# Kernel optimization log

Hardware: AMD Instinct MI355X
Metric: run time of the kernel (lower is better)

Reference implementation:

```python
import jax, jax.numpy as jnp
import numpy as np

B, L, D, H, NL, NR, FF = 4, 512, 1024, 8, 2, 37, 4096
DH = D // H  # 128, relation embedding dim (shared across heads, per RAT-SQL)


def layer_norm(x, g, b, eps=1e-5):
    m = jnp.mean(x, axis=-1, keepdims=True)
    v = jnp.mean(jnp.square(x - m), axis=-1, keepdims=True)
    return (x - m) * jax.lax.rsqrt(v + eps) * g + b


def setup_inputs() -> dict:
    key = jax.random.key(0)
    ks = iter(jax.random.split(key, 24))

    def p(shape, scale=0.02):
        return jax.random.normal(next(ks), shape, jnp.float32) * scale

    return {
        "x": jax.random.normal(next(ks), (B, L, D), jnp.float32),
        "relations": jax.random.randint(next(ks), (B, L, L), 0, NR),
        "Wq": p((NL, D, D)), "bq": jnp.zeros((NL, D), jnp.float32),
        "Wk": p((NL, D, D)), "bk": jnp.zeros((NL, D), jnp.float32),
        "Wv": p((NL, D, D)), "bv": jnp.zeros((NL, D), jnp.float32),
        "Wo": p((NL, D, D)), "bo": jnp.zeros((NL, D), jnp.float32),
        "rel_k": p((NL, NR, DH)), "rel_v": p((NL, NR, DH)),
        "W1": p((NL, D, FF)), "b1": jnp.zeros((NL, FF), jnp.float32),
        "W2": p((NL, FF, D)), "b2": jnp.zeros((NL, D), jnp.float32),
        "ln1_g": jnp.ones((NL, D), jnp.float32), "ln1_b": jnp.zeros((NL, D), jnp.float32),
        "ln2_g": jnp.ones((NL, D), jnp.float32), "ln2_b": jnp.zeros((NL, D), jnp.float32),
        "lnf_g": jnp.ones((D,), jnp.float32), "lnf_b": jnp.zeros((D,), jnp.float32),
    }


def reference(x, relations, Wq, bq, Wk, bk, Wv, bv, Wo, bo, rel_k, rel_v,
              W1, b1, W2, b2, ln1_g, ln1_b, ln2_g, ln2_b, lnf_g, lnf_b):
    scale = jnp.float32(1.0 / np.sqrt(DH))

    def split_heads(t):  # [B,L,D] -> [B,H,L,DH]
        return t.reshape(B, L, H, DH).transpose(0, 2, 1, 3)

    for l in range(NL):
        # --- relation-aware multi-head attention (pre-norm sublayer) ---
        h = layer_norm(x, ln1_g[l], ln1_b[l])
        q = split_heads(h @ Wq[l] + bq[l])
        k = split_heads(h @ Wk[l] + bk[l])
        v = split_heads(h @ Wv[l] + bv[l])
        rk = rel_k[l][relations]  # [B,L,L,DH] gathered relation key embeddings
        rv = rel_v[l][relations]  # [B,L,L,DH]
        scores = (jnp.einsum('bhid,bhjd->bhij', q, k)
                  + jnp.einsum('bhid,bijd->bhij', q, rk)) * scale
        attn = jax.nn.softmax(scores, axis=-1)  # [B,H,L,L]
        o = (jnp.einsum('bhij,bhjd->bhid', attn, v)
             + jnp.einsum('bhij,bijd->bhid', attn, rv))
        o = o.transpose(0, 2, 1, 3).reshape(B, L, D) @ Wo[l] + bo[l]
        x = x + o
        # --- feed-forward sublayer (pre-norm) ---
        h2 = layer_norm(x, ln2_g[l], ln2_b[l])
        x = x + jax.nn.relu(h2 @ W1[l] + b1[l]) @ W2[l] + b2[l]
    return layer_norm(x, lnf_g, lnf_b)
```

## Files before the change

kernel.cpp:

```cpp
#include <hip/hip_runtime.h>

#define Bdim 4
#define Ldim 512
#define Ddim 1024
#define Hdim 8
#define NLdim 2
#define NRdim 37
#define FFdim 4096
#define DHdim 128
#define ROWS 2048

using bf16x8 = __attribute__((ext_vector_type(8))) short;
using s16x4  = __attribute__((ext_vector_type(4))) short;
using s16x8  = __attribute__((ext_vector_type(8))) short;
using f32x4  = __attribute__((ext_vector_type(4))) float;

struct HL { short h, l; };
__device__ __forceinline__ HL splitf(float f) {
    HL r;
    unsigned u = __float_as_uint(f);
    unsigned rh = (u + 0x7FFFu + ((u >> 16) & 1u)) >> 16;
    r.h = (short)rh;
    float res = f - __uint_as_float(rh << 16);
    unsigned v = __float_as_uint(res);
    r.l = (short)((v + 0x7FFFu + ((v >> 16) & 1u)) >> 16);
    return r;
}

__device__ __forceinline__ size_t ssa_off(int row, int k, int KK) {
    return (size_t)row * KK + (k & ~63) + (((((k >> 3) & 7) ^ (row & 7))) << 3) + (k & 7);
}

__device__ __forceinline__ void gload16(const void* g, void* l) {
    __builtin_amdgcn_global_load_lds(
        (const __attribute__((address_space(1))) void*)g,
        (__attribute__((address_space(3))) void*)l, 16, 0, 0);
}

template<bool SPLIT>
__global__ __launch_bounds__(256) void ln_kernel(
    const float* __restrict__ x, const float* __restrict__ g,
    const float* __restrict__ beta, float* __restrict__ outf,
    short* __restrict__ oh, short* __restrict__ ol)
{
    int row = blockIdx.x;
    int t = threadIdx.x;
    const float4* xr = (const float4*)(x + (size_t)row * Ddim);
    float4 v = xr[t];
    float s  = v.x + v.y + v.z + v.w;
    float ss = v.x*v.x + v.y*v.y + v.z*v.z + v.w*v.w;
    #pragma unroll
    for (int off = 32; off; off >>= 1) {
        s  += __shfl_down(s, off);
        ss += __shfl_down(ss, off);
    }
    __shared__ float rs[4], rss[4], stat[2];
    int wave = t >> 6, lane = t & 63;
    if (lane == 0) { rs[wave] = s; rss[wave] = ss; }
    __syncthreads();
    if (t == 0) {
        float a = rs[0] + rs[1] + rs[2] + rs[3];
        float b = rss[0] + rss[1] + rss[2] + rss[3];
        float mean = a * (1.0f / Ddim);
        float var  = b * (1.0f / Ddim) - mean * mean;
        stat[0] = mean;
        stat[1] = rsqrtf(var + 1e-5f);
    }
    __syncthreads();
    float mean = stat[0], inv = stat[1];
    float4 gv = ((const float4*)g)[t];
    float4 bv = ((const float4*)beta)[t];
    float4 o;
    o.x = (v.x - mean) * inv * gv.x + bv.x;
    o.y = (v.y - mean) * inv * gv.y + bv.y;
    o.z = (v.z - mean) * inv * gv.z + bv.z;
    o.w = (v.w - mean) * inv * gv.w + bv.w;
    if (SPLIT) {
        int d = t * 4;
        size_t off = ssa_off(row, d, Ddim);
        HL a0 = splitf(o.x), a1 = splitf(o.y), a2 = splitf(o.z), a3 = splitf(o.w);
        s16x4 hv, lv;
        hv[0] = a0.h; hv[1] = a1.h; hv[2] = a2.h; hv[3] = a3.h;
        lv[0] = a0.l; lv[1] = a1.l; lv[2] = a2.l; lv[3] = a3.l;
        *(s16x4*)&oh[off] = hv;
        *(s16x4*)&ol[off] = lv;
    } else {
        ((float4*)(outf + (size_t)row * Ddim))[t] = o;
    }
}

__global__ __launch_bounds__(256) void prep_w(
    const float* __restrict__ W, short* __restrict__ oh, short* __restrict__ ol,
    int N, int logN)
{
    int gi = blockIdx.x * 256 + threadIdx.x;
    int n = gi & (N - 1);
    int rest = gi >> logN;
    int g = rest & 7, kt = rest >> 3;
    const float* src = W + ((size_t)(kt * 64 + g * 8)) * N + n;
    s16x8 h8, l8;
    #pragma unroll
    for (int j = 0; j < 8; ++j) {
        HL a = splitf(src[(size_t)j * N]);
        h8[j] = a.h; l8[j] = a.l;
    }
    size_t off = ((size_t)kt * N + n) * 64 + (((g ^ (n & 7))) << 3);
    *(s16x8*)&oh[off] = h8;
    *(s16x8*)&ol[off] = l8;
}

struct G3 {
    const short* Wh[3]; const short* Wl[3];
    const float* bias[3];
    float* outf[3];
    short* oh[3]; short* ol[3];
};

template<bool RES, bool RELU, bool SPLIT>
__global__ __launch_bounds__(256) void gemm3(
    const short* __restrict__ Ahi, const short* __restrict__ Alo,
    const float* __restrict__ res, G3 gp, int N, int K)
{
    __shared__ __align__(16) short As_h[128 * 64];
    __shared__ __align__(16) short As_l[128 * 64];
    __shared__ __align__(16) short Ws_h[64 * 64];
    __shared__ __align__(16) short Ws_l[64 * 64];

    int z = blockIdx.z;
    const short* Wh = gp.Wh[z];
    const short* Wl = gp.Wl[z];
    const float* bias = gp.bias[z];

    int t = threadIdx.x, wid = t >> 6, lane = t & 63;
    int bm = blockIdx.y * 128, bn = blockIdx.x * 64;
    int wr = wid >> 1, wc = wid & 1;

    f32x4 acc[4][2];
    #pragma unroll
    for (int m = 0; m < 4; ++m)
        #pragma unroll
        for (int n = 0; n < 2; ++n)
            acc[m][n] = (f32x4)(0.f);

    int nkt = K >> 6;
    int l8r = lane >> 3, l8c = lane & 7;

    for (int kt = 0; kt < nkt; ++kt) {
        size_t kof = (size_t)kt * 64 + l8c * 8;
        #pragma unroll
        for (int qq = 0; qq < 4; ++qq) {
            int rb = wid * 32 + qq * 8;
            gload16(Ahi + (size_t)(bm + rb + l8r) * K + kof, &As_h[rb * 64]);
            gload16(Alo + (size_t)(bm + rb + l8r) * K + kof, &As_l[rb * 64]);
        }
        size_t wbase = (size_t)kt * N * 64;
        #pragma unroll
        for (int qq = 0; qq < 2; ++qq) {
            int nb = wid * 16 + qq * 8;
            gload16(Wh + wbase + (size_t)(bn + nb + l8r) * 64 + l8c * 8, &Ws_h[nb * 64]);
            gload16(Wl + wbase + (size_t)(bn + nb + l8r) * 64 + l8c * 8, &Ws_l[nb * 64]);
        }
        __syncthreads();
        #pragma unroll
        for (int ks = 0; ks < 2; ++ks) {
            int kg = ks * 4 + (lane >> 4);
            int sw = (kg ^ (lane & 7)) << 3;
            bf16x8 ah[4], al[4], bh[2], bl[2];
            #pragma unroll
            for (int m = 0; m < 4; ++m) {
                int off = (wr * 64 + m * 16 + (lane & 15)) * 64 + sw;
                ah[m] = *(const bf16x8*)&As_h[off];
                al[m] = *(const bf16x8*)&As_l[off];
            }
            #pragma unroll
            for (int n = 0; n < 2; ++n) {
                int off = (wc * 32 + n * 16 + (lane & 15)) * 64 + sw;
                bh[n] = *(const bf16x8*)&Ws_h[off];
                bl[n] = *(const bf16x8*)&Ws_l[off];
            }
            #pragma unroll
            for (int m = 0; m < 4; ++m)
                #pragma unroll
                for (int n = 0; n < 2; ++n) {
                    acc[m][n] = __builtin_amdgcn_mfma_f32_16x16x32_bf16(ah[m], bh[n], acc[m][n], 0, 0, 0);
                    acc[m][n] = __builtin_amdgcn_mfma_f32_16x16x32_bf16(ah[m], bl[n], acc[m][n], 0, 0, 0);
                    acc[m][n] = __builtin_amdgcn_mfma_f32_16x16x32_bf16(al[m], bh[n], acc[m][n], 0, 0, 0);
                }
        }
        __syncthreads();
    }

    int r0 = (lane >> 4) << 2, cl = lane & 15;
    #pragma unroll
    for (int m = 0; m < 4; ++m) {
        #pragma unroll
        for (int n = 0; n < 2; ++n) {
            int col = bn + wc * 32 + n * 16 + cl;
            float bia = bias[col];
            #pragma unroll
            for (int j = 0; j < 4; ++j) {
                int row = bm + wr * 64 + m * 16 + r0 + j;
                float val = acc[m][n][j] + bia;
                if (RES) val += res[(size_t)row * N + col];
                if (RELU) val = fmaxf(val, 0.f);
                if (SPLIT) {
                    HL a = splitf(val);
                    size_t o = ssa_off(row, col, N);
                    gp.oh[z][o] = a.h;
                    gp.ol[z][o] = a.l;
                } else {
                    gp.outf[z][(size_t)row * N + col] = val;
                }
            }
        }
    }
}

__global__ __launch_bounds__(256) void qr_kernel(
    const float* __restrict__ q, const float* __restrict__ relk,
    float* __restrict__ qr)
{
    __shared__ __align__(16) float qrow[Ddim];
    __shared__ float rkT[DHdim][NRdim + 3];
    int bi = blockIdx.x, t = threadIdx.x;
    ((float4*)qrow)[t] = ((const float4*)(q + (size_t)bi * Ddim))[t];
    for (int idx = t; idx < NRdim * DHdim; idx += 256) {
        int r = idx >> 7, d = idx & 127;
        rkT[d][r] = relk[idx];
    }
    __syncthreads();
    for (int o = t; o < Hdim * NRdim; o += 256) {
        int h = o / NRdim, r = o - h * NRdim;
        const float* qp = qrow + h * DHdim;
        float acc = 0.f;
        #pragma unroll 4
        for (int d = 0; d < DHdim; ++d)
            acc = fmaf(qp[d], rkT[d][r], acc);
        qr[(size_t)bi * (Hdim * NRdim) + o] = acc;
    }
}

__global__ __launch_bounds__(256) void attn_kernel(
    const float* __restrict__ q, const float* __restrict__ k,
    const float* __restrict__ v, const int* __restrict__ relations,
    const float* __restrict__ qr, const float* __restrict__ relv,
    short* __restrict__ o_hi, short* __restrict__ o_lo)
{
    __shared__ __align__(16) float Qs[32][132];
    __shared__ __align__(16) float Ks[32][132];
    __shared__ __align__(16) float Vs[32][132];
    __shared__ float Ps[32][36];
    __shared__ float aw[32][40];

    int t = threadIdx.x;
    int blk = blockIdx.x;
    int it = blk & 15, bh = blk >> 4;
    int h = bh & 7, b = bh >> 3;
    int i0 = it * 32;
    int r = t >> 3, q8 = t & 7;
    int row_g = b * Ldim + i0 + r;

    const float* qrow = q + (size_t)row_g * Ddim + h * DHdim;
    #pragma unroll
    for (int c = 0; c < 4; ++c)
        *(float4*)&Qs[r][q8 * 16 + c * 4] = *(const float4*)&qrow[q8 * 16 + c * 4];
    for (int idx = t; idx < 32 * 40; idx += 256) ((float*)aw)[idx] = 0.f;

    const int*   relp = relations + (size_t)row_g * Ldim;
    const float* qrp  = qr + (size_t)row_g * (Hdim * NRdim) + h * NRdim;

    float4 oc0 = make_float4(0,0,0,0), oc1 = oc0, oc2 = oc0, oc3 = oc0;
    float mrun = -1e30f, lsum = 0.f;
    const float scale = 0.08838834764831845f;

    for (int jt = 0; jt < 16; ++jt) {
        int j0 = jt * 32;
        __syncthreads();
        const float* krow = k + (size_t)(b * Ldim + j0 + r) * Ddim + h * DHdim;
        const float* vrow = v + (size_t)(b * Ldim + j0 + r) * Ddim + h * DHdim;
        #pragma unroll
        for (int c = 0; c < 4; ++c) {
            *(float4*)&Ks[r][q8 * 16 + c * 4] = *(const float4*)&krow[q8 * 16 + c * 4];
            *(float4*)&Vs[r][q8 * 16 + c * 4] = *(const float4*)&vrow[q8 * 16 + c * 4];
        }
        __syncthreads();

        float s0 = 0.f, s1 = 0.f, s2 = 0.f, s3 = 0.f;
        #pragma unroll 8
        for (int dq = 0; dq < 32; ++dq) {
            float4 qv = *(const float4*)&Qs[r][dq * 4];
            float4 k0 = *(const float4*)&Ks[q8     ][dq * 4];
            float4 k1 = *(const float4*)&Ks[q8 +  8][dq * 4];
            float4 k2 = *(const float4*)&Ks[q8 + 16][dq * 4];
            float4 k3 = *(const float4*)&Ks[q8 + 24][dq * 4];
            s0 = fmaf(qv.x, k0.x, s0); s0 = fmaf(qv.y, k0.y, s0); s0 = fmaf(qv.z, k0.z, s0); s0 = fmaf(qv.w, k0.w, s0);
            s1 = fmaf(qv.x, k1.x, s1); s1 = fmaf(qv.y, k1.y, s1); s1 = fmaf(qv.z, k1.z, s1); s1 = fmaf(qv.w, k1.w, s1);
            s2 = fmaf(qv.x, k2.x, s2); s2 = fmaf(qv.y, k2.y, s2); s2 = fmaf(qv.z, k2.z, s2); s2 = fmaf(qv.w, k2.w, s2);
            s3 = fmaf(qv.x, k3.x, s3); s3 = fmaf(qv.y, k3.y, s3); s3 = fmaf(qv.z, k3.z, s3); s3 = fmaf(qv.w, k3.w, s3);
        }
        int rel0 = relp[j0 + q8];
        int rel1 = relp[j0 + q8 + 8];
        int rel2 = relp[j0 + q8 + 16];
        int rel3 = relp[j0 + q8 + 24];
        s0 = (s0 + qrp[rel0]) * scale;
        s1 = (s1 + qrp[rel1]) * scale;
        s2 = (s2 + qrp[rel2]) * scale;
        s3 = (s3 + qrp[rel3]) * scale;

        float mt = fmaxf(fmaxf(s0, s1), fmaxf(s2, s3));
        mt = fmaxf(mt, __shfl_xor(mt, 1));
        mt = fmaxf(mt, __shfl_xor(mt, 2));
        mt = fmaxf(mt, __shfl_xor(mt, 4));
        float mnew = fmaxf(mrun, mt);
        float corr = __expf(mrun - mnew);
        mrun = mnew;
        float p0 = __expf(s0 - mnew);
        float p1 = __expf(s1 - mnew);
        float p2 = __expf(s2 - mnew);
        float p3 = __expf(s3 - mnew);
        lsum = lsum * corr + (p0 + p1 + p2 + p3);
        oc0.x *= corr; oc0.y *= corr; oc0.z *= corr; oc0.w *= corr;
        oc1.x *= corr; oc1.y *= corr; oc1.z *= corr; oc1.w *= corr;
        oc2.x *= corr; oc2.y *= corr; oc2.z *= corr; oc2.w *= corr;
        oc3.x *= corr; oc3.y *= corr; oc3.z *= corr; oc3.w *= corr;
        for (int ri = q8; ri < NRdim; ri += 8) aw[r][ri] *= corr;
        atomicAdd(&aw[r][rel0], p0);
        atomicAdd(&aw[r][rel1], p1);
        atomicAdd(&aw[r][rel2], p2);
        atomicAdd(&aw[r][rel3], p3);
        Ps[r][q8]      = p0;
        Ps[r][q8 + 8]  = p1;
        Ps[r][q8 + 16] = p2;
        Ps[r][q8 + 24] = p3;

        #pragma unroll 4
        for (int j = 0; j < 32; ++j) {
            float p = Ps[r][j];
            float4 v0 = *(const float4*)&Vs[j][(q8     ) * 4];
            float4 v1 = *(const float4*)&Vs[j][(q8 +  8) * 4];
            float4 v2 = *(const float4*)&Vs[j][(q8 + 16) * 4];
            float4 v3 = *(const float4*)&Vs[j][(q8 + 24) * 4];
            oc0.x = fmaf(p, v0.x, oc0.x); oc0.y = fmaf(p, v0.y, oc0.y); oc0.z = fmaf(p, v0.z, oc0.z); oc0.w = fmaf(p, v0.w, oc0.w);
            oc1.x = fmaf(p, v1.x, oc1.x); oc1.y = fmaf(p, v1.y, oc1.y); oc1.z = fmaf(p, v1.z, oc1.z); oc1.w = fmaf(p, v1.w, oc1.w);
            oc2.x = fmaf(p, v2.x, oc2.x); oc2.y = fmaf(p, v2.y, oc2.y); oc2.z = fmaf(p, v2.z, oc2.z); oc2.w = fmaf(p, v2.w, oc2.w);
            oc3.x = fmaf(p, v3.x, oc3.x); oc3.y = fmaf(p, v3.y, oc3.y); oc3.z = fmaf(p, v3.z, oc3.z); oc3.w = fmaf(p, v3.w, oc3.w);
        }
    }

    lsum += __shfl_xor(lsum, 1);
    lsum += __shfl_xor(lsum, 2);
    lsum += __shfl_xor(lsum, 4);
    float inv = 1.0f / lsum;

    float4 o20 = make_float4(0,0,0,0), o21 = o20, o22 = o20, o23 = o20;
    for (int rp = 0; rp < NRdim; ++rp) {
        float w = aw[r][rp];
        const float4* rv = (const float4*)(relv + (size_t)rp * DHdim);
        float4 a0 = rv[q8], a1 = rv[q8 + 8], a2 = rv[q8 + 16], a3 = rv[q8 + 24];
        o20.x = fmaf(w, a0.x, o20.x); o20.y = fmaf(w, a0.y, o20.y); o20.z = fmaf(w, a0.z, o20.z); o20.w = fmaf(w, a0.w, o20.w);
        o21.x = fmaf(w, a1.x, o21.x); o21.y = fmaf(w, a1.y, o21.y); o21.z = fmaf(w, a1.z, o21.z); o21.w = fmaf(w, a1.w, o21.w);
        o22.x = fmaf(w, a2.x, o22.x); o22.y = fmaf(w, a2.y, o22.y); o22.z = fmaf(w, a2.z, o22.z); o22.w = fmaf(w, a2.w, o22.w);
        o23.x = fmaf(w, a3.x, o23.x); o23.y = fmaf(w, a3.y, o23.y); o23.z = fmaf(w, a3.z, o23.z); o23.w = fmaf(w, a3.w, o23.w);
    }

    float4 vals[4];
    vals[0].x = (oc0.x + o20.x) * inv; vals[0].y = (oc0.y + o20.y) * inv; vals[0].z = (oc0.z + o20.z) * inv; vals[0].w = (oc0.w + o20.w) * inv;
    vals[1].x = (oc1.x + o21.x) * inv; vals[1].y = (oc1.y + o21.y) * inv; vals[1].z = (oc1.z + o21.z) * inv; vals[1].w = (oc1.w + o21.w) * inv;
    vals[2].x = (oc2.x + o22.x) * inv; vals[2].y = (oc2.y + o22.y) * inv; vals[2].z = (oc2.z + o22.z) * inv; vals[2].w = (oc2.w + o22.w) * inv;
    vals[3].x = (oc3.x + o23.x) * inv; vals[3].y = (oc3.y + o23.y) * inv; vals[3].z = (oc3.z + o23.z) * inv; vals[3].w = (oc3.w + o23.w) * inv;
    #pragma unroll
    for (int c = 0; c < 4; ++c) {
        int d = (q8 + 8 * c) * 4;
        int kk = h * DHdim + d;
        size_t off = ssa_off(row_g, kk, Ddim);
        HL a0 = splitf(vals[c].x), a1 = splitf(vals[c].y),
           a2 = splitf(vals[c].z), a3 = splitf(vals[c].w);
        s16x4 hv, lv;
        hv[0] = a0.h; hv[1] = a1.h; hv[2] = a2.h; hv[3] = a3.h;
        lv[0] = a0.l; lv[1] = a1.l; lv[2] = a2.l; lv[3] = a3.l;
        *(s16x4*)&o_hi[off] = hv;
        *(s16x4*)&o_lo[off] = lv;
    }
}

extern "C" void kernel_launch(void* const* d_in, const int* in_sizes, int n_in,
                              void* d_out, int out_size, void* d_ws, size_t ws_size,
                              hipStream_t stream)
{
    const float* x     = (const float*)d_in[0];
    const int*   rel   = (const int*)  d_in[1];
    const float* Wq    = (const float*)d_in[2];
    const float* bq    = (const float*)d_in[3];
    const float* Wk    = (const float*)d_in[4];
    const float* bk    = (const float*)d_in[5];
    const float* Wv    = (const float*)d_in[6];
    const float* bv    = (const float*)d_in[7];
    const float* Wo    = (const float*)d_in[8];
    const float* bo    = (const float*)d_in[9];
    const float* rel_k = (const float*)d_in[10];
    const float* rel_v = (const float*)d_in[11];
    const float* W1    = (const float*)d_in[12];
    const float* b1    = (const float*)d_in[13];
    const float* W2    = (const float*)d_in[14];
    const float* b2    = (const float*)d_in[15];
    const float* ln1_g = (const float*)d_in[16];
    const float* ln1_b = (const float*)d_in[17];
    const float* ln2_g = (const float*)d_in[18];
    const float* ln2_b = (const float*)d_in[19];
    const float* lnf_g = (const float*)d_in[20];
    const float* lnf_b = (const float*)d_in[21];

    const size_t MB = 1u << 20;
    char* w = (char*)d_ws;
    float* xbuf = (float*)w;
    short* h_hi = (short*)(w + 8 * MB);
    short* h_lo = (short*)(w + 12 * MB);
    char*  regC = w + 16 * MB;
    float* qb   = (float*)regC;
    float* kb   = (float*)(regC + 8 * MB);
    float* vb   = (float*)(regC + 16 * MB);
    float* qrb  = (float*)(regC + 24 * MB);
    short* ffh  = (short*)regC;
    short* ffl  = (short*)(regC + 16 * MB);
    short* o_hi = (short*)(w + 48 * MB);
    short* o_lo = (short*)(w + 52 * MB);
    short* wbh  = (short*)(w + 56 * MB);
    short* wbl  = (short*)(w + 64 * MB);

    (void)hipMemcpyAsync(xbuf, x, sizeof(float) * (size_t)ROWS * Ddim,
                         hipMemcpyDeviceToDevice, stream);

    dim3 blk(256);
    const size_t MSH = 1048576;

    for (int l = 0; l < NLdim; ++l) {
        const float* Wq_l = Wq + (size_t)l * Ddim * Ddim;
        const float* Wk_l = Wk + (size_t)l * Ddim * Ddim;
        const float* Wv_l = Wv + (size_t)l * Ddim * Ddim;
        const float* Wo_l = Wo + (size_t)l * Ddim * Ddim;
        const float* W1_l = W1 + (size_t)l * Ddim * FFdim;
        const float* W2_l = W2 + (size_t)l * FFdim * Ddim;
        const float* rk_l = rel_k + (size_t)l * NRdim * DHdim;
        const float* rv_l = rel_v + (size_t)l * NRdim * DHdim;

        ln_kernel<true><<<ROWS, blk, 0, stream>>>(xbuf, ln1_g + l * Ddim, ln1_b + l * Ddim,
                                                  nullptr, h_hi, h_lo);
        prep_w<<<512, blk, 0, stream>>>(Wq_l, wbh, wbl, Ddim, 10);
        prep_w<<<512, blk, 0, stream>>>(Wk_l, wbh + MSH, wbl + MSH, Ddim, 10);
        prep_w<<<512, blk, 0, stream>>>(Wv_l, wbh + 2 * MSH, wbl + 2 * MSH, Ddim, 10);
        {
            G3 g{};
            g.Wh[0] = wbh;           g.Wl[0] = wbl;
            g.Wh[1] = wbh + MSH;     g.Wl[1] = wbl + MSH;
            g.Wh[2] = wbh + 2 * MSH; g.Wl[2] = wbl + 2 * MSH;
            g.bias[0] = bq + l * Ddim; g.bias[1] = bk + l * Ddim; g.bias[2] = bv + l * Ddim;
            g.outf[0] = qb; g.outf[1] = kb; g.outf[2] = vb;
            gemm3<false, false, false><<<dim3(16, 16, 3), blk, 0, stream>>>(
                h_hi, h_lo, nullptr, g, Ddim, Ddim);
        }
        qr_kernel<<<ROWS, blk, 0, stream>>>(qb, rk_l, qrb);
        attn_kernel<<<512, blk, 0, stream>>>(qb, kb, vb, rel, qrb, rv_l, o_hi, o_lo);
        prep_w<<<512, blk, 0, stream>>>(Wo_l, wbh, wbl, Ddim, 10);
        {
            G3 g{};
            g.Wh[0] = wbh; g.Wl[0] = wbl;
            g.bias[0] = bo + l * Ddim;
            g.outf[0] = xbuf;
            gemm3<true, false, false><<<dim3(16, 16, 1), blk, 0, stream>>>(
                o_hi, o_lo, xbuf, g, Ddim, Ddim);
        }
        ln_kernel<true><<<ROWS, blk, 0, stream>>>(xbuf, ln2_g + l * Ddim, ln2_b + l * Ddim,
                                                  nullptr, h_hi, h_lo);
        prep_w<<<2048, blk, 0, stream>>>(W1_l, wbh, wbl, FFdim, 12);
        {
            G3 g{};
            g.Wh[0] = wbh; g.Wl[0] = wbl;
            g.bias[0] = b1 + l * FFdim;
            g.oh[0] = ffh; g.ol[0] = ffl;
            gemm3<false, true, true><<<dim3(64, 16, 1), blk, 0, stream>>>(
                h_hi, h_lo, nullptr, g, FFdim, Ddim);
        }
        prep_w<<<2048, blk, 0, stream>>>(W2_l, wbh, wbl, Ddim, 10);
        {
            G3 g{};
            g.Wh[0] = wbh; g.Wl[0] = wbl;
            g.bias[0] = b2 + l * Ddim;
            g.outf[0] = xbuf;
            gemm3<true, false, false><<<dim3(16, 16, 1), blk, 0, stream>>>(
                ffh, ffl, xbuf, g, Ddim, FFdim);
        }
    }
    ln_kernel<false><<<ROWS, blk, 0, stream>>>(xbuf, lnf_g, lnf_b, (float*)d_out,
                                               nullptr, nullptr);
}
```

Baseline: 1.081 ms.

## Move attention QK and PV to bf16 MFMA with split-bf16 Q/K/V layouts

Replaces the scalar fp32 attention kernel with an MFMA-based one. The QKV GEMM now writes Q and K as hi/lo bf16 pairs in a swizzled layout and writes V transposed and tiled for the PV product. The kernel splits the KV range across wave pairs, loads tiles with global_load_lds, and merges the two partial softmax states at the end. K is used only at its hi part and P is rounded to bf16, which lowers precision. The aim is to remove FMA-bound scalar attention and cut fp32 Q/K/V memory traffic.

Result: faster. 938.6 us (-13.2%).

```diff
diff --git a/kernel.cpp b/kernel.cpp
--- a/kernel.cpp
+++ b/kernel.cpp
@@ -14,6 +14,7 @@
 using s16x4  = __attribute__((ext_vector_type(4))) short;
 using s16x8  = __attribute__((ext_vector_type(8))) short;
 using f32x4  = __attribute__((ext_vector_type(4))) float;
+using u32 = unsigned int;
 
 struct HL { short h, l; };
 __device__ __forceinline__ HL splitf(float f) {
@@ -25,6 +26,9 @@
     unsigned v = __float_as_uint(res);
     r.l = (short)((v + 0x7FFFu + ((v >> 16) & 1u)) >> 16);
     return r;
+}
+__device__ __forceinline__ float b2f(short s) {
+    return __uint_as_float(((unsigned)(unsigned short)s) << 16);
 }
 
 __device__ __forceinline__ size_t ssa_off(int row, int k, int KK) {
@@ -114,6 +118,7 @@
     const float* bias[3];
     float* outf[3];
     short* oh[3]; short* ol[3];
+    short* vt[3];
 };
 
 template<bool RES, bool RELU, bool SPLIT>
@@ -191,6 +196,7 @@
     }
 
     int r0 = (lane >> 4) << 2, cl = lane & 15;
+    short* vtp = gp.vt[z];
     #pragma unroll
     for (int m = 0; m < 4; ++m) {
         #pragma unroll
@@ -203,7 +209,18 @@
                 float val = acc[m][n][j] + bia;
                 if (RES) val += res[(size_t)row * N + col];
                 if (RELU) val = fmaxf(val, 0.f);
-                if (SPLIT) {
+                if (vtp) {
+                    HL a = splitf(val);
+                    int bb = row >> 9, jj2 = row & 511;
+                    int hh = col >> 7, d = col & 127;
+                    int bhI = bb * Hdim + hh;
+                    int jt16 = jj2 >> 5;
+                    int chi = (jj2 >> 3) & 3;
+                    int ph = chi ^ (d & 7);
+                    size_t base = (((size_t)bhI * 128 + d) * 16 + jt16) * 64;
+                    vtp[base + ph * 8 + (jj2 & 7)] = a.h;
+                    vtp[base + (ph ^ 4) * 8 + (jj2 & 7)] = a.l;
+                } else if (SPLIT) {
                     HL a = splitf(val);
                     size_t o = ssa_off(row, col, N);
                     gp.oh[z][o] = a.h;
@@ -217,13 +234,22 @@
 }
 
 __global__ __launch_bounds__(256) void qr_kernel(
-    const float* __restrict__ q, const float* __restrict__ relk,
-    float* __restrict__ qr)
+    const short* __restrict__ qh, const short* __restrict__ ql,
+    const float* __restrict__ relk, float* __restrict__ qr)
 {
     __shared__ __align__(16) float qrow[Ddim];
     __shared__ float rkT[DHdim][NRdim + 3];
     int bi = blockIdx.x, t = threadIdx.x;
-    ((float4*)qrow)[t] = ((const float4*)(q + (size_t)bi * Ddim))[t];
+    {
+        int d0 = t * 4;
+        int g = (d0 >> 3) & 7;
+        int pos = g ^ (bi & 7);
+        size_t off = (size_t)bi * Ddim + (d0 & ~63) + pos * 8 + (d0 & 7);
+        s16x4 hv = *(const s16x4*)&qh[off];
+        s16x4 lv = *(const s16x4*)&ql[off];
+        #pragma unroll
+        for (int e = 0; e < 4; ++e) qrow[d0 + e] = b2f(hv[e]) + b2f(lv[e]);
+    }
     for (int idx = t; idx < NRdim * DHdim; idx += 256) {
         int r = idx >> 7, d = idx & 127;
         rkT[d][r] = relk[idx];
@@ -240,146 +266,189 @@
     }
 }
 
-__global__ __launch_bounds__(256) void attn_kernel(
-    const float* __restrict__ q, const float* __restrict__ k,
-    const float* __restrict__ v, const int* __restrict__ relations,
-    const float* __restrict__ qr, const float* __restrict__ relv,
+__global__ __launch_bounds__(256) void attn_mfma(
+    const short* __restrict__ qh, const short* __restrict__ ql,
+    const short* __restrict__ kh, const short* __restrict__ vt,
+    const int* __restrict__ relations, const float* __restrict__ qr,
+    const float* __restrict__ relv,
     short* __restrict__ o_hi, short* __restrict__ o_lo)
 {
-    __shared__ __align__(16) float Qs[32][132];
-    __shared__ __align__(16) float Ks[32][132];
-    __shared__ __align__(16) float Vs[32][132];
-    __shared__ float Ps[32][36];
-    __shared__ float aw[32][40];
+    __shared__ __align__(16) short Kh_s[2][32][128];
+    __shared__ __align__(16) short Vt_s[2][128][64];
+    __shared__ float aw_s[4][16][NRdim + 3];
+    __shared__ float mg_s[2][16][2];
 
     int t = threadIdx.x;
+    int wid = t >> 6, lane = t & 63;
+    int q = lane & 15, g = lane >> 4;
+    int rowhalf = wid & 1, kvhalf = wid >> 1;
+
     int blk = blockIdx.x;
     int it = blk & 15, bh = blk >> 4;
     int h = bh & 7, b = bh >> 3;
     int i0 = it * 32;
-    int r = t >> 3, q8 = t & 7;
-    int row_g = b * Ldim + i0 + r;
-
-    const float* qrow = q + (size_t)row_g * Ddim + h * DHdim;
+    int bL = b * Ldim;
+    int rowg = bL + i0 + rowhalf * 16 + q;
+
+    for (int idx = t; idx < 4 * 16 * (NRdim + 3); idx += 256)
+        ((float*)aw_s)[idx] = 0.f;
+
+    bf16x8 qhf[4], qlf[4];
     #pragma unroll
-    for (int c = 0; c < 4; ++c)
-        *(float4*)&Qs[r][q8 * 16 + c * 4] = *(const float4*)&qrow[q8 * 16 + c * 4];
-    for (int idx = t; idx < 32 * 40; idx += 256) ((float*)aw)[idx] = 0.f;
-
-    const int*   relp = relations + (size_t)row_g * Ldim;
-    const float* qrp  = qr + (size_t)row_g * (Hdim * NRdim) + h * NRdim;
-
-    float4 oc0 = make_float4(0,0,0,0), oc1 = oc0, oc2 = oc0, oc3 = oc0;
+    for (int ks = 0; ks < 4; ++ks) {
+        int c = (ks & 1) * 4 + g;
+        size_t off = (size_t)rowg * Ddim + (h * 2 + (ks >> 1)) * 64
+                   + ((c ^ (rowg & 7)) * 8);
+        qhf[ks] = *(const bf16x8*)&qh[off];
+        qlf[ks] = *(const bf16x8*)&ql[off];
+    }
+
+    const int*   relp = relations + (size_t)rowg * Ldim;
+    const float* qrp  = qr + (size_t)rowg * (Hdim * NRdim) + h * NRdim;
+    const float scale = 0.08838834764831845f;
+
+    f32x4 acc_o[8];
+    #pragma unroll
+    for (int dt = 0; dt < 8; ++dt) acc_o[dt] = (f32x4)(0.f);
     float mrun = -1e30f, lsum = 0.f;
-    const float scale = 0.08838834764831845f;
-
-    for (int jt = 0; jt < 16; ++jt) {
-        int j0 = jt * 32;
+    float* awrow = &aw_s[wid][q][0];
+
+    for (int rr = 0; rr < 8; ++rr) {
+        #pragma unroll
+        for (int uu = 0; uu < 12; ++uu) {
+            int u = wid * 12 + uu;
+            if (u < 16) {
+                int s = u >> 3, i = u & 7;
+                const short* src = kh
+                    + (size_t)(bL + s * 256 + rr * 32 + 4 * i + (lane >> 4)) * Ddim
+                    + h * 128 + (lane & 15) * 8;
+                gload16(src, &Kh_s[s][4 * i][0]);
+            } else {
+                int v = u - 16;
+                int s = v >> 4, i = v & 15;
+                const short* src = vt
+                    + (((size_t)bh * 128 + 8 * i + (lane >> 3)) * 16 + s * 8 + rr) * 64
+                    + (lane & 7) * 8;
+                gload16(src, &Vt_s[s][8 * i][0]);
+            }
+        }
         __syncthreads();
-        const float* krow = k + (size_t)(b * Ldim + j0 + r) * Ddim + h * DHdim;
-        const float* vrow = v + (size_t)(b * Ldim + j0 + r) * Ddim + h * DHdim;
-        #pragma unroll
-        for (int c = 0; c < 4; ++c) {
-            *(float4*)&Ks[r][q8 * 16 + c * 4] = *(const float4*)&krow[q8 * 16 + c * 4];
-            *(float4*)&Vs[r][q8 * 16 + c * 4] = *(const float4*)&vrow[q8 * 16 + c * 4];
-        }
-        __syncthreads();
-
-        float s0 = 0.f, s1 = 0.f, s2 = 0.f, s3 = 0.f;
-        #pragma unroll 8
-        for (int dq = 0; dq < 32; ++dq) {
-            float4 qv = *(const float4*)&Qs[r][dq * 4];
-            float4 k0 = *(const float4*)&Ks[q8     ][dq * 4];
-            float4 k1 = *(const float4*)&Ks[q8 +  8][dq * 4];
-            float4 k2 = *(const float4*)&Ks[q8 + 16][dq * 4];
-            float4 k3 = *(const float4*)&Ks[q8 + 24][dq * 4];
-            s0 = fmaf(qv.x, k0.x, s0); s0 = fmaf(qv.y, k0.y, s0); s0 = fmaf(qv.z, k0.z, s0); s0 = fmaf(qv.w, k0.w, s0);
-            s1 = fmaf(qv.x, k1.x, s1); s1 = fmaf(qv.y, k1.y, s1); s1 = fmaf(qv.z, k1.z, s1); s1 = fmaf(qv.w, k1.w, s1);
-            s2 = fmaf(qv.x, k2.x, s2); s2 = fmaf(qv.y, k2.y, s2); s2 = fmaf(qv.z, k2.z, s2); s2 = fmaf(qv.w, k2.w, s2);
-            s3 = fmaf(qv.x, k3.x, s3); s3 = fmaf(qv.y, k3.y, s3); s3 = fmaf(qv.z, k3.z, s3); s3 = fmaf(qv.w, k3.w, s3);
-        }
-        int rel0 = relp[j0 + q8];
-        int rel1 = relp[j0 + q8 + 8];
-        int rel2 = relp[j0 + q8 + 16];
-        int rel3 = relp[j0 + q8 + 24];
-        s0 = (s0 + qrp[rel0]) * scale;
-        s1 = (s1 + qrp[rel1]) * scale;
-        s2 = (s2 + qrp[rel2]) * scale;
-        s3 = (s3 + qrp[rel3]) * scale;
-
-        float mt = fmaxf(fmaxf(s0, s1), fmaxf(s2, s3));
-        mt = fmaxf(mt, __shfl_xor(mt, 1));
-        mt = fmaxf(mt, __shfl_xor(mt, 2));
-        mt = fmaxf(mt, __shfl_xor(mt, 4));
+
+        int st = kvhalf;
+        int j0 = kvhalf * 256 + rr * 32;
+
+        f32x4 sAcc[2];
+        sAcc[0] = (f32x4)(0.f); sAcc[1] = (f32x4)(0.f);
+        #pragma unroll
+        for (int Mt = 0; Mt < 2; ++Mt)
+            #pragma unroll
+            for (int ks = 0; ks < 4; ++ks) {
+                int pos = (((ks & 1) * 4 + g) ^ (q & 7));
+                bf16x8 kv = *(const bf16x8*)&Kh_s[st][Mt * 16 + q][(ks >> 1) * 64 + pos * 8];
+                sAcc[Mt] = __builtin_amdgcn_mfma_f32_16x16x32_bf16(kv, qhf[ks], sAcc[Mt], 0, 0, 0);
+                sAcc[Mt] = __builtin_amdgcn_mfma_f32_16x16x32_bf16(kv, qlf[ks], sAcc[Mt], 0, 0, 0);
+            }
+
+        float sv[8]; int r8[8];
+        #pragma unroll
+        for (int Mt = 0; Mt < 2; ++Mt)
+            #pragma unroll
+            for (int jj = 0; jj < 4; ++jj) {
+                int kcol = Mt * 16 + g * 4 + jj;
+                int rel = relp[j0 + kcol];
+                r8[Mt * 4 + jj] = rel;
+                sv[Mt * 4 + jj] = (sAcc[Mt][jj] + qrp[rel]) * scale;
+            }
+
+        float mt = sv[0];
+        #pragma unroll
+        for (int k = 1; k < 8; ++k) mt = fmaxf(mt, sv[k]);
+        mt = fmaxf(mt, __shfl_xor(mt, 16));
+        mt = fmaxf(mt, __shfl_xor(mt, 32));
         float mnew = fmaxf(mrun, mt);
         float corr = __expf(mrun - mnew);
         mrun = mnew;
-        float p0 = __expf(s0 - mnew);
-        float p1 = __expf(s1 - mnew);
-        float p2 = __expf(s2 - mnew);
-        float p3 = __expf(s3 - mnew);
-        lsum = lsum * corr + (p0 + p1 + p2 + p3);
-        oc0.x *= corr; oc0.y *= corr; oc0.z *= corr; oc0.w *= corr;
-        oc1.x *= corr; oc1.y *= corr; oc1.z *= corr; oc1.w *= corr;
-        oc2.x *= corr; oc2.y *= corr; oc2.z *= corr; oc2.w *= corr;
-        oc3.x *= corr; oc3.y *= corr; oc3.z *= corr; oc3.w *= corr;
-        for (int ri = q8; ri < NRdim; ri += 8) aw[r][ri] *= corr;
-        atomicAdd(&aw[r][rel0], p0);
-        atomicAdd(&aw[r][rel1], p1);
-        atomicAdd(&aw[r][rel2], p2);
-        atomicAdd(&aw[r][rel3], p3);
-        Ps[r][q8]      = p0;
-        Ps[r][q8 + 8]  = p1;
-        Ps[r][q8 + 16] = p2;
-        Ps[r][q8 + 24] = p3;
-
-        #pragma unroll 4
-        for (int j = 0; j < 32; ++j) {
-            float p = Ps[r][j];
-            float4 v0 = *(const float4*)&Vs[j][(q8     ) * 4];
-            float4 v1 = *(const float4*)&Vs[j][(q8 +  8) * 4];
-            float4 v2 = *(const float4*)&Vs[j][(q8 + 16) * 4];
-            float4 v3 = *(const float4*)&Vs[j][(q8 + 24) * 4];
-            oc0.x = fmaf(p, v0.x, oc0.x); oc0.y = fmaf(p, v0.y, oc0.y); oc0.z = fmaf(p, v0.z, oc0.z); oc0.w = fmaf(p, v0.w, oc0.w);
-            oc1.x = fmaf(p, v1.x, oc1.x); oc1.y = fmaf(p, v1.y, oc1.y); oc1.z = fmaf(p, v1.z, oc1.z); oc1.w = fmaf(p, v1.w, oc1.w);
-            oc2.x = fmaf(p, v2.x, oc2.x); oc2.y = fmaf(p, v2.y, oc2.y); oc2.z = fmaf(p, v2.z, oc2.z); oc2.w = fmaf(p, v2.w, oc2.w);
-            oc3.x = fmaf(p, v3.x, oc3.x); oc3.y = fmaf(p, v3.y, oc3.y); oc3.z = fmaf(p, v3.z, oc3.z); oc3.w = fmaf(p, v3.w, oc3.w);
-        }
-    }
-
-    lsum += __shfl_xor(lsum, 1);
-    lsum += __shfl_xor(lsum, 2);
-    lsum += __shfl_xor(lsum, 4);
-    float inv = 1.0f / lsum;
-
-    float4 o20 = make_float4(0,0,0,0), o21 = o20, o22 = o20, o23 = o20;
-    for (int rp = 0; rp < NRdim; ++rp) {
-        float w = aw[r][rp];
-        const float4* rv = (const float4*)(relv + (size_t)rp * DHdim);
-        float4 a0 = rv[q8], a1 = rv[q8 + 8], a2 = rv[q8 + 16], a3 = rv[q8 + 24];
-        o20.x = fmaf(w, a0.x, o20.x); o20.y = fmaf(w, a0.y, o20.y); o20.z = fmaf(w, a0.z, o20.z); o20.w = fmaf(w, a0.w, o20.w);
-        o21.x = fmaf(w, a1.x, o21.x); o21.y = fmaf(w, a1.y, o21.y); o21.z = fmaf(w, a1.z, o21.z); o21.w = fmaf(w, a1.w, o21.w);
-        o22.x = fmaf(w, a2.x, o22.x); o22.y = fmaf(w, a2.y, o22.y); o22.z = fmaf(w, a2.z, o22.z); o22.w = fmaf(w, a2.w, o22.w);
-        o23.x = fmaf(w, a3.x, o23.x); o23.y = fmaf(w, a3.y, o23.y); o23.z = fmaf(w, a3.z, o23.z); o23.w = fmaf(w, a3.w, o23.w);
-    }
-
-    float4 vals[4];
-    vals[0].x = (oc0.x + o20.x) * inv; vals[0].y = (oc0.y + o20.y) * inv; vals[0].z = (oc0.z + o20.z) * inv; vals[0].w = (oc0.w + o20.w) * inv;
-    vals[1].x = (oc1.x + o21.x) * inv; vals[1].y = (oc1.y + o21.y) * inv; vals[1].z = (oc1.z + o21.z) * inv; vals[1].w = (oc1.w + o21.w) * inv;
-    vals[2].x = (oc2.x + o22.x) * inv; vals[2].y = (oc2.y + o22.y) * inv; vals[2].z = (oc2.z + o22.z) * inv; vals[2].w = (oc2.w + o22.w) * inv;
-    vals[3].x = (oc3.x + o23.x) * inv; vals[3].y = (oc3.y + o23.y) * inv; vals[3].z = (oc3.z + o23.z) * inv; vals[3].w = (oc3.w + o23.w) * inv;
-    #pragma unroll
-    for (int c = 0; c < 4; ++c) {
-        int d = (q8 + 8 * c) * 4;
-        int kk = h * DHdim + d;
-        size_t off = ssa_off(row_g, kk, Ddim);
-        HL a0 = splitf(vals[c].x), a1 = splitf(vals[c].y),
-           a2 = splitf(vals[c].z), a3 = splitf(vals[c].w);
-        s16x4 hv, lv;
-        hv[0] = a0.h; hv[1] = a1.h; hv[2] = a2.h; hv[3] = a3.h;
-        lv[0] = a0.l; lv[1] = a1.l; lv[2] = a2.l; lv[3] = a3.l;
-        *(s16x4*)&o_hi[off] = hv;
-        *(s16x4*)&o_lo[off] = lv;
+        float p[8]; float psum = 0.f;
+        #pragma unroll
+        for (int k = 0; k < 8; ++k) { p[k] = __expf(sv[k] - mnew); psum += p[k]; }
+        lsum = lsum * corr + psum;
+        #pragma unroll
+        for (int dt = 0; dt < 8; ++dt) acc_o[dt] *= corr;
+        int rbase = g * 10, nr = (g == 3) ? 7 : 10;
+        for (int ri = 0; ri < nr; ++ri) awrow[rbase + ri] *= corr;
+        #pragma unroll
+        for (int k = 0; k < 8; ++k) atomicAdd(&awrow[r8[k]], p[k]);
+
+        u32 pk[4];
+        asm("v_cvt_pk_bf16_f32 %0, %1, %2" : "=v"(pk[0]) : "v"(p[0]), "v"(p[1]));
+        asm("v_cvt_pk_bf16_f32 %0, %1, %2" : "=v"(pk[1]) : "v"(p[2]), "v"(p[3]));
+        asm("v_cvt_pk_bf16_f32 %0, %1, %2" : "=v"(pk[2]) : "v"(p[4]), "v"(p[5]));
+        asm("v_cvt_pk_bf16_f32 %0, %1, %2" : "=v"(pk[3]) : "v"(p[6]), "v"(p[7]));
+        union { u32 u[4]; bf16x8 v; } pb;
+        int mtsel = g >> 1;
+        #pragma unroll
+        for (int i = 0; i < 4; ++i) {
+            int src = q + 16 * ((2 * g + (i >> 1)) & 3);
+            u32 lo = __shfl(pk[i & 1], src);
+            u32 hi = __shfl(pk[2 + (i & 1)], src);
+            pb.u[i] = mtsel ? hi : lo;
+        }
+        bf16x8 pfrag = pb.v;
+
+        #pragma unroll
+        for (int dt = 0; dt < 8; ++dt) {
+            int ph = g ^ (q & 7);
+            bf16x8 vh = *(const bf16x8*)&Vt_s[st][dt * 16 + q][ph * 8];
+            bf16x8 vl = *(const bf16x8*)&Vt_s[st][dt * 16 + q][(ph ^ 4) * 8];
+            acc_o[dt] = __builtin_amdgcn_mfma_f32_16x16x32_bf16(vh, pfrag, acc_o[dt], 0, 0, 0);
+            acc_o[dt] = __builtin_amdgcn_mfma_f32_16x16x32_bf16(vl, pfrag, acc_o[dt], 0, 0, 0);
+        }
+        __syncthreads();
+    }
+
+    lsum += __shfl_xor(lsum, 16);
+    lsum += __shfl_xor(lsum, 32);
+    for (int r = 0; r < NRdim; ++r) {
+        float w = awrow[r];
+        #pragma unroll
+        for (int dt = 0; dt < 8; ++dt) {
+            float4 rv = *(const float4*)&relv[r * DHdim + dt * 16 + g * 4];
+            acc_o[dt][0] = fmaf(w, rv.x, acc_o[dt][0]);
+            acc_o[dt][1] = fmaf(w, rv.y, acc_o[dt][1]);
+            acc_o[dt][2] = fmaf(w, rv.z, acc_o[dt][2]);
+            acc_o[dt][3] = fmaf(w, rv.w, acc_o[dt][3]);
+        }
+    }
+
+    float* mrg = (float*)Vt_s;
+    if (kvhalf == 1) {
+        float* mo = mrg + rowhalf * 2048;
+        #pragma unroll
+        for (int dt = 0; dt < 8; ++dt)
+            #pragma unroll
+            for (int jj = 0; jj < 4; ++jj)
+                mo[q * 128 + dt * 16 + g * 4 + jj] = acc_o[dt][jj];
+        if (g == 0) { mg_s[rowhalf][q][0] = mrun; mg_s[rowhalf][q][1] = lsum; }
+    }
+    __syncthreads();
+    if (kvhalf == 0) {
+        float m2 = mg_s[rowhalf][q][0], l2 = mg_s[rowhalf][q][1];
+        float mf = fmaxf(mrun, m2);
+        float a1 = __expf(mrun - mf), a2 = __expf(m2 - mf);
+        float inv = 1.0f / (lsum * a1 + l2 * a2);
+        float* mo = mrg + rowhalf * 2048;
+        #pragma unroll
+        for (int dt = 0; dt < 8; ++dt)
+            #pragma unroll
+            for (int jj = 0; jj < 4; ++jj) {
+                int d = dt * 16 + g * 4 + jj;
+                float O = acc_o[dt][jj] * a1 + mo[q * 128 + d] * a2;
+                float out = O * inv;
+                HL a = splitf(out);
+                size_t off = ssa_off(rowg, h * DHdim + d, Ddim);
+                o_hi[off] = a.h;
+                o_lo[off] = a.l;
+            }
     }
 }
 
@@ -415,17 +484,18 @@
     float* xbuf = (float*)w;
     short* h_hi = (short*)(w + 8 * MB);
     short* h_lo = (short*)(w + 12 * MB);
-    char*  regC = w + 16 * MB;
-    float* qb   = (float*)regC;
-    float* kb   = (float*)(regC + 8 * MB);
-    float* vb   = (float*)(regC + 16 * MB);
-    float* qrb  = (float*)(regC + 24 * MB);
-    short* ffh  = (short*)regC;
-    short* ffl  = (short*)(regC + 16 * MB);
+    short* qhB  = (short*)(w + 16 * MB);
+    short* qlB  = (short*)(w + 20 * MB);
+    short* khB  = (short*)(w + 24 * MB);
+    short* klB  = (short*)(w + 28 * MB);
+    short* vtB  = (short*)(w + 32 * MB);
+    float* qrb  = (float*)(w + 40 * MB);
     short* o_hi = (short*)(w + 48 * MB);
     short* o_lo = (short*)(w + 52 * MB);
     short* wbh  = (short*)(w + 56 * MB);
     short* wbl  = (short*)(w + 64 * MB);
+    short* ffh  = (short*)(w + 16 * MB);
+    short* ffl  = (short*)(w + 32 * MB);
 
     (void)hipMemcpyAsync(xbuf, x, sizeof(float) * (size_t)ROWS * Ddim,
                          hipMemcpyDeviceToDevice, stream);
@@ -454,12 +524,14 @@
             g.Wh[1] = wbh + MSH;     g.Wl[1] = wbl + MSH;
             g.Wh[2] = wbh + 2 * MSH; g.Wl[2] = wbl + 2 * MSH;
             g.bias[0] = bq + l * Ddim; g.bias[1] = bk + l * Ddim; g.bias[2] = bv + l * Ddim;
-            g.outf[0] = qb; g.outf[1] = kb; g.outf[2] = vb;
-            gemm3<false, false, false><<<dim3(16, 16, 3), blk, 0, stream>>>(
+            g.oh[0] = qhB; g.ol[0] = qlB;
+            g.oh[1] = khB; g.ol[1] = klB;
+            g.vt[2] = vtB;
+            gemm3<false, false, true><<<dim3(16, 16, 3), blk, 0, stream>>>(
                 h_hi, h_lo, nullptr, g, Ddim, Ddim);
         }
-        qr_kernel<<<ROWS, blk, 0, stream>>>(qb, rk_l, qrb);
-        attn_kernel<<<512, blk, 0, stream>>>(qb, kb, vb, rel, qrb, rv_l, o_hi, o_lo);
+        qr_kernel<<<ROWS, blk, 0, stream>>>(qhB, qlB, rk_l, qrb);
+        attn_mfma<<<512, blk, 0, stream>>>(qhB, qlB, khB, vtB, rel, qrb, rv_l, o_hi, o_lo);
         prep_w<<<512, blk, 0, stream>>>(Wo_l, wbh, wbl, Ddim, 10);
         {
             G3 g{};
```
